# Kernel tuning notes

Hardware: AMD Instinct MI355X
Metric: run time of the kernel (lower is better)

The kernel has to match this reference:

```python
import jax, jax.numpy as jnp
import numpy as np

N_NODES = 100000
N_EDGES = 1250000
D = 64
N_LAYERS = 4


def setup_inputs() -> dict:
    key = jax.random.key(0)
    ks = jax.random.split(key, 6)
    x = jax.random.normal(ks[0], (N_NODES, D), dtype=jnp.float32)
    edge_index = jax.random.randint(ks[1], (2, N_EDGES), 0, N_NODES, dtype=jnp.int64)
    s = 1.0 / np.sqrt(D)
    # PyG SAGEConv per layer: lin_l (applied to aggregated neighbors, with bias)
    # and lin_r (applied to self features, no bias). All layers are 64->64, so stack.
    Wl = jax.random.uniform(ks[2], (N_LAYERS, D, D), dtype=jnp.float32, minval=-s, maxval=s)
    bl = jax.random.uniform(ks[3], (N_LAYERS, D), dtype=jnp.float32, minval=-s, maxval=s)
    Wr = jax.random.uniform(ks[4], (N_LAYERS, D, D), dtype=jnp.float32, minval=-s, maxval=s)
    return {"x": x, "edge_index": edge_index, "Wl": Wl, "bl": bl, "Wr": Wr}


def reference(x, edge_index, Wl, bl, Wr):
    src = edge_index[0]  # message source: x_j
    dst = edge_index[1]  # aggregate at target node
    h = x
    for i in range(N_LAYERS):
        msg = h[src]  # [E, D] irregular gather
        agg = jax.ops.segment_max(msg, dst, num_segments=N_NODES)  # max-pool aggregation
        agg = jnp.where(jnp.isneginf(agg), 0.0, agg)  # empty segments -> 0 (PyG convention)
        h = jax.nn.relu(agg @ Wl[i] + bl[i] + h @ Wr[i])
    return h
```

## Files before the change

kernel.cpp:

```cpp
#include <hip/hip_runtime.h>
#include <hip/hip_fp16.h>
#include <stdint.h>

#define NN 100000
#define NE 1250000
#define DD 64
#define NL 4

#define NPART3 64
#define PSIZE3 1563
#define TILE4 1024
#define NTB ((NE / 4 + TILE4 - 1) / TILE4)
#define SCANA_N (NPART3 * NTB)
#define SRCBITS 17

#define MB2 64
#define L2BLOCKS ((NN + MB2 - 1) / MB2)
#define APAD 136
#define CPADH 72
#define CPADF 68

typedef _Float16 half8 __attribute__((ext_vector_type(8)));
typedef _Float16 half2v __attribute__((ext_vector_type(2)));
typedef float floatx4 __attribute__((ext_vector_type(4)));
typedef int intx4 __attribute__((ext_vector_type(4)));

__device__ __forceinline__ float2 h2f2(unsigned u) {
    __half2 h = *reinterpret_cast<__half2*>(&u);
    return __half22float2(h);
}
__device__ __forceinline__ unsigned f2h2(float a, float b) {
    __half2 h = __floats2half2_rn(a, b);
    return *reinterpret_cast<unsigned*>(&h);
}
__device__ __forceinline__ unsigned umax2(unsigned a, unsigned b) {
    half2v x = *reinterpret_cast<half2v*>(&a);
    half2v y = *reinterpret_cast<half2v*>(&b);
    half2v r = __builtin_elementwise_max(x, y);
    return *reinterpret_cast<unsigned*>(&r);
}

__global__ __launch_bounds__(256) void cast_kernel(const float* __restrict__ x,
                                                   __half* __restrict__ hh) {
    int i = blockIdx.x * 256 + threadIdx.x;
    float4 v = ((const float4*)x)[i];
    uint2 u;
    u.x = f2h2(v.x, v.y);
    u.y = f2h2(v.z, v.w);
    ((uint2*)hh)[i] = u;
}

__global__ __launch_bounds__(256) void countA_kernel(const int* __restrict__ dst,
                                                     int* __restrict__ blockcnt) {
    __shared__ int cnt[NPART3];
    int tid = threadIdx.x;
    if (tid < NPART3) cnt[tid] = 0;
    __syncthreads();
    int b = blockIdx.x;
    #pragma unroll
    for (int r = 0; r < 4; ++r) {
        int i4 = b * TILE4 + r * 256 + tid;
        if (i4 < NE / 4) {
            intx4 d = __builtin_nontemporal_load(&((const intx4*)dst)[i4]);
            atomicAdd(&cnt[(unsigned)d.x / PSIZE3], 1);
            atomicAdd(&cnt[(unsigned)d.y / PSIZE3], 1);
            atomicAdd(&cnt[(unsigned)d.z / PSIZE3], 1);
            atomicAdd(&cnt[(unsigned)d.w / PSIZE3], 1);
        }
    }
    __syncthreads();
    if (tid < NPART3) blockcnt[tid * NTB + b] = cnt[tid];
}

__global__ __launch_bounds__(1024) void scanA_kernel(int* __restrict__ blockcnt) {
    __shared__ int sm[1024];
    int tid = threadIdx.x;
    int base = tid * 20;
    int e[20];
    int s = 0;
    #pragma unroll
    for (int j = 0; j < 20; ++j) {
        e[j] = (base + j < SCANA_N) ? blockcnt[base + j] : 0;
        s += e[j];
    }
    sm[tid] = s;
    __syncthreads();
    for (int off = 1; off < 1024; off <<= 1) {
        int v = (tid >= off) ? sm[tid - off] : 0;
        __syncthreads();
        sm[tid] += v;
        __syncthreads();
    }
    int run = sm[tid] - s;
    #pragma unroll
    for (int j = 0; j < 20; ++j) {
        if (base + j < SCANA_N) {
            blockcnt[base + j] = run;
            run += e[j];
        }
    }
}

__global__ __launch_bounds__(256) void scatterA_kernel(const int* __restrict__ src,
                                                       const int* __restrict__ dst,
                                                       const int* __restrict__ blockcnt,
                                                       int* __restrict__ ebufP) {
    __shared__ int cur[NPART3];
    int tid = threadIdx.x;
    int b = blockIdx.x;
    if (tid < NPART3) cur[tid] = blockcnt[tid * NTB + b];
    __syncthreads();
    #pragma unroll
    for (int r = 0; r < 4; ++r) {
        int i4 = b * TILE4 + r * 256 + tid;
        if (i4 < NE / 4) {
            intx4 d = __builtin_nontemporal_load(&((const intx4*)dst)[i4]);
            intx4 s = __builtin_nontemporal_load(&((const intx4*)src)[i4]);
            int part, p;
            part = (unsigned)d.x / PSIZE3; p = atomicAdd(&cur[part], 1);
            ebufP[p] = ((d.x - part * PSIZE3) << SRCBITS) | s.x;
            part = (unsigned)d.y / PSIZE3; p = atomicAdd(&cur[part], 1);
            ebufP[p] = ((d.y - part * PSIZE3) << SRCBITS) | s.y;
            part = (unsigned)d.z / PSIZE3; p = atomicAdd(&cur[part], 1);
            ebufP[p] = ((d.z - part * PSIZE3) << SRCBITS) | s.z;
            part = (unsigned)d.w / PSIZE3; p = atomicAdd(&cur[part], 1);
            ebufP[p] = ((d.w - part * PSIZE3) << SRCBITS) | s.w;
        }
    }
}

__global__ __launch_bounds__(1024) void fillD_kernel(const int* __restrict__ ebufP,
                                                     const int* __restrict__ blockcnt,
                                                     int* __restrict__ row_start,
                                                     int* __restrict__ csr) {
    __shared__ int cnt[PSIZE3];
    __shared__ int localstart[PSIZE3];
    __shared__ int partial[1024];
    int part = blockIdx.x;
    int tid = threadIdx.x;
    int nbase = part * PSIZE3;
    int base = blockcnt[part * NTB];
    int hi = (part < NPART3 - 1) ? blockcnt[(part + 1) * NTB] : NE;

    for (int j = tid; j < PSIZE3; j += 1024) cnt[j] = 0;
    __syncthreads();

    for (int i = base + tid; i < hi; i += 1024)
        atomicAdd(&cnt[(unsigned)ebufP[i] >> SRCBITS], 1);
    __syncthreads();

    int j0 = tid * 2;
    int e0 = (j0 < PSIZE3) ? cnt[j0] : 0;
    int e1 = (j0 + 1 < PSIZE3) ? cnt[j0 + 1] : 0;
    int s = e0 + e1;
    partial[tid] = s;
    __syncthreads();
    for (int off = 1; off < 1024; off <<= 1) {
        int v = (tid >= off) ? partial[tid - off] : 0;
        __syncthreads();
        partial[tid] += v;
        __syncthreads();
    }
    int run = partial[tid] - s;
    if (j0 < PSIZE3) localstart[j0] = run;
    if (j0 + 1 < PSIZE3) localstart[j0 + 1] = run + e0;
    __syncthreads();

    int nmax = NN - nbase; if (nmax > PSIZE3) nmax = PSIZE3;
    for (int j = tid; j < nmax; j += 1024)
        row_start[nbase + j] = base + localstart[j];
    if (part == NPART3 - 1 && tid == 0) row_start[NN] = NE;

    for (int j = tid; j < PSIZE3; j += 1024) cnt[j] = 0;
    __syncthreads();

    for (int i = base + tid; i < hi; i += 1024) {
        int p = ebufP[i];
        int dl = (unsigned)p >> SRCBITS;
        int local = atomicAdd(&cnt[dl], 1);
        csr[base + localstart[dl] + local] = p & ((1 << SRCBITS) - 1);
    }
}

__global__ __launch_bounds__(256) void agg_kernel(const __half* __restrict__ hh,
                                                  const int* __restrict__ row_start,
                                                  const int* __restrict__ csr,
                                                  __half* __restrict__ aggh) {
    int tid = threadIdx.x;
    int wv = tid >> 6;
    int lane = tid & 63;
    int g = lane >> 3;
    int c8 = (lane & 7) * 8;
    int n = blockIdx.x * 4 + wv;
    int base = row_start[n];
    int cnt = row_start[n + 1] - base;

    if (cnt > 0) {
        int clampi = cnt - 1;
        int pre = (lane <= clampi) ? lane : clampi;
        int idx = csr[base + pre];

        uint4 acc = make_uint4(0xFC00FC00u, 0xFC00FC00u, 0xFC00FC00u, 0xFC00FC00u);
        int kmax = (cnt < 64) ? cnt : 64;
        for (int k = 0; k < kmax; k += 16) {
            int k0 = k + g;
            int k1 = k + g + 8;
            int s0 = __shfl(idx, (k0 <= clampi) ? k0 : clampi, 64);
            int s1 = __shfl(idx, (k1 <= clampi) ? k1 : clampi, 64);
            if (k0 < cnt) {
                uint4 u0 = *(const uint4*)&hh[(size_t)s0 * DD + c8];
                acc.x = umax2(acc.x, u0.x);
                acc.y = umax2(acc.y, u0.y);
                acc.z = umax2(acc.z, u0.z);
                acc.w = umax2(acc.w, u0.w);
            }
            if (k1 < cnt) {
                uint4 u1 = *(const uint4*)&hh[(size_t)s1 * DD + c8];
                acc.x = umax2(acc.x, u1.x);
                acc.y = umax2(acc.y, u1.y);
                acc.z = umax2(acc.z, u1.z);
                acc.w = umax2(acc.w, u1.w);
            }
        }
        for (int k = 64 + g; k < cnt; k += 8) {
            int s = csr[base + k];
            uint4 u = *(const uint4*)&hh[(size_t)s * DD + c8];
            acc.x = umax2(acc.x, u.x);
            acc.y = umax2(acc.y, u.y);
            acc.z = umax2(acc.z, u.z);
            acc.w = umax2(acc.w, u.w);
        }
        #pragma unroll
        for (int off = 8; off <= 32; off <<= 1) {
            acc.x = umax2(acc.x, (unsigned)__shfl_xor((int)acc.x, off, 64));
            acc.y = umax2(acc.y, (unsigned)__shfl_xor((int)acc.y, off, 64));
            acc.z = umax2(acc.z, (unsigned)__shfl_xor((int)acc.z, off, 64));
            acc.w = umax2(acc.w, (unsigned)__shfl_xor((int)acc.w, off, 64));
        }
        if (lane < 8) *(uint4*)&aggh[(size_t)n * DD + c8] = acc;
    } else {
        if (lane < 8) {
            uint4 z = make_uint4(0, 0, 0, 0);
            *(uint4*)&aggh[(size_t)n * DD + c8] = z;
        }
    }
}

__global__ __launch_bounds__(256, 4) void layer_mfma_kernel(
        const __half* __restrict__ aggh,
        __half* __restrict__ hh,
        float* __restrict__ hout,
        const float* __restrict__ Wl,
        const float* __restrict__ bl,
        const float* __restrict__ Wr,
        int last) {
    __shared__ char smem[2 * MB2 * APAD * 2];
    _Float16* a_s  = (_Float16*)smem;
    _Float16* bt_s = (_Float16*)(smem + MB2 * APAD * 2);

    int tid = threadIdx.x;
    int lane = tid & 63;
    int w = tid >> 6;
    int node0 = blockIdx.x * MB2;

    #pragma unroll
    for (int i = 0; i < 4; ++i) {
        int idx = i * 256 + tid;
        int r = idx >> 4;
        int c4 = idx & 15;
        int node = node0 + r; if (node > NN - 1) node = NN - 1;
        const __half* srcp = (c4 < 8) ? (aggh + (size_t)node * DD + c4 * 8)
                                      : (hh + (size_t)node * DD + (c4 - 8) * 8);
        uint4 v = *(const uint4*)srcp;
        *(uint4*)&a_s[r * APAD + c4 * 8] = v;
    }
    {
        int n = tid & 63;
        int kb = tid >> 6;
        #pragma unroll
        for (int kk = 0; kk < 32; ++kk) {
            int k = kb * 32 + kk;
            float wv = (k < 64) ? Wl[k * DD + n] : Wr[(k - 64) * DD + n];
            bt_s[n * APAD + k] = (_Float16)wv;
        }
    }
    __syncthreads();

    floatx4 acc[4];
    #pragma unroll
    for (int nt = 0; nt < 4; ++nt) acc[nt] = (floatx4){0.f, 0.f, 0.f, 0.f};
    int m = lane & 15;
    int q = lane >> 4;

    #pragma unroll
    for (int ks = 0; ks < 4; ++ks) {
        half8 af = *(half8*)&a_s[(w * 16 + m) * APAD + q * 8 + ks * 32];
        #pragma unroll
        for (int nt = 0; nt < 4; ++nt) {
            half8 bf = *(half8*)&bt_s[(nt * 16 + m) * APAD + q * 8 + ks * 32];
            acc[nt] = __builtin_amdgcn_mfma_f32_16x16x32_f16(af, bf, acc[nt], 0, 0, 0);
        }
    }
    __syncthreads();

    _Float16* ch = (_Float16*)smem;
    float*    cf = (float*)(smem + MB2 * CPADH * 2);

    #pragma unroll
    for (int nt = 0; nt < 4; ++nt) {
        int col = nt * 16 + m;
        float b = bl[col];
        #pragma unroll
        for (int r = 0; r < 4; ++r) {
            int rowl = w * 16 + q * 4 + r;
            float o = fmaxf(acc[nt][r] + b, 0.0f);
            ch[rowl * CPADH + col] = (_Float16)o;
            if (last) cf[rowl * CPADF + col] = o;
        }
    }
    __syncthreads();

    #pragma unroll
    for (int i = 0; i < 2; ++i) {
        int idx = i * 256 + tid;
        int r = idx >> 3;
        int c4 = idx & 7;
        int node = node0 + r;
        if (node < NN) {
            uint4 v = *(uint4*)&ch[r * CPADH + c4 * 8];
            *(uint4*)&hh[(size_t)node * DD + c4 * 8] = v;
        }
    }
    if (last) {
        #pragma unroll
        for (int i = 0; i < 4; ++i) {
            int idx = i * 256 + tid;
            int r = idx >> 4;
            int c4 = idx & 15;
            int node = node0 + r;
            if (node < NN) {
                float4 v = *(float4*)&cf[r * CPADF + c4 * 4];
                *(float4*)&hout[(size_t)node * DD + c4 * 4] = v;
            }
        }
    }
}

extern "C" void kernel_launch(void* const* d_in, const int* in_sizes, int n_in,
                              void* d_out, int out_size, void* d_ws, size_t ws_size,
                              hipStream_t stream) {
    const float* x  = (const float*)d_in[0];
    const int*   ei = (const int*)d_in[1];
    const float* Wl = (const float*)d_in[2];
    const float* bl = (const float*)d_in[3];
    const float* Wr = (const float*)d_in[4];
    float* h = (float*)d_out;

    const int* src = ei;
    const int* dst = ei + NE;

    char* ws = (char*)d_ws;
    __half* aggh     = (__half*)ws;  ws += (size_t)NN * DD * sizeof(__half);
    __half* hh       = (__half*)ws;  ws += (size_t)NN * DD * sizeof(__half);
    int* row_start   = (int*)ws;     ws += (size_t)(NN + 16) * sizeof(int);
    int* blockcnt    = (int*)ws;     ws += (size_t)(SCANA_N + 16) * sizeof(int);
    int* csr         = (int*)ws;

    int* ebufP = (int*)aggh;

    cast_kernel<<<(NN * DD / 4) / 256, 256, 0, stream>>>(x, hh);

    countA_kernel<<<NTB, 256, 0, stream>>>(dst, blockcnt);
    scanA_kernel<<<1, 1024, 0, stream>>>(blockcnt);
    scatterA_kernel<<<NTB, 256, 0, stream>>>(src, dst, blockcnt, ebufP);
    fillD_kernel<<<NPART3, 1024, 0, stream>>>(ebufP, blockcnt, row_start, csr);

    for (int l = 0; l < NL; ++l) {
        agg_kernel<<<NN / 4, 256, 0, stream>>>(hh, row_start, csr, aggh);
        layer_mfma_kernel<<<L2BLOCKS, 256, 0, stream>>>(
            aggh, hh, h, Wl + (size_t)l * DD * DD, bl + (size_t)l * DD, Wr + (size_t)l * DD * DD,
            (l == NL - 1) ? 1 : 0);
    }
}
```

Baseline: 317.5 us.

## Fuse max-aggregation gather into the MFMA layer kernel with ping-pong buffers

Removes the separate aggregation kernel: each wave of the layer kernel now gathers and max-reduces neighbor features for 16 nodes directly into shared memory before the MFMA. The fp16 hidden state ping-pongs between two buffers so reads and writes don't race. This cuts the intermediate aggregation buffer's global write and read and one launch per layer. In exchange, each wave handles its 16 nodes one after another, with far fewer blocks in flight, which can hurt latency hiding for the irregular gathers.

```diff
diff --git a/kernel.cpp b/kernel.cpp
--- a/kernel.cpp
+++ b/kernel.cpp
@@ -25,10 +25,6 @@
 typedef float floatx4 __attribute__((ext_vector_type(4)));
 typedef int intx4 __attribute__((ext_vector_type(4)));
 
-__device__ __forceinline__ float2 h2f2(unsigned u) {
-    __half2 h = *reinterpret_cast<__half2*>(&u);
-    return __half22float2(h);
-}
 __device__ __forceinline__ unsigned f2h2(float a, float b) {
     __half2 h = __floats2half2_rn(a, b);
     return *reinterpret_cast<unsigned*>(&h);
@@ -182,74 +178,12 @@
     }
 }
 
-__global__ __launch_bounds__(256) void agg_kernel(const __half* __restrict__ hh,
-                                                  const int* __restrict__ row_start,
-                                                  const int* __restrict__ csr,
-                                                  __half* __restrict__ aggh) {
-    int tid = threadIdx.x;
-    int wv = tid >> 6;
-    int lane = tid & 63;
-    int g = lane >> 3;
-    int c8 = (lane & 7) * 8;
-    int n = blockIdx.x * 4 + wv;
-    int base = row_start[n];
-    int cnt = row_start[n + 1] - base;
-
-    if (cnt > 0) {
-        int clampi = cnt - 1;
-        int pre = (lane <= clampi) ? lane : clampi;
-        int idx = csr[base + pre];
-
-        uint4 acc = make_uint4(0xFC00FC00u, 0xFC00FC00u, 0xFC00FC00u, 0xFC00FC00u);
-        int kmax = (cnt < 64) ? cnt : 64;
-        for (int k = 0; k < kmax; k += 16) {
-            int k0 = k + g;
-            int k1 = k + g + 8;
-            int s0 = __shfl(idx, (k0 <= clampi) ? k0 : clampi, 64);
-            int s1 = __shfl(idx, (k1 <= clampi) ? k1 : clampi, 64);
-            if (k0 < cnt) {
-                uint4 u0 = *(const uint4*)&hh[(size_t)s0 * DD + c8];
-                acc.x = umax2(acc.x, u0.x);
-                acc.y = umax2(acc.y, u0.y);
-                acc.z = umax2(acc.z, u0.z);
-                acc.w = umax2(acc.w, u0.w);
-            }
-            if (k1 < cnt) {
-                uint4 u1 = *(const uint4*)&hh[(size_t)s1 * DD + c8];
-                acc.x = umax2(acc.x, u1.x);
-                acc.y = umax2(acc.y, u1.y);
-                acc.z = umax2(acc.z, u1.z);
-                acc.w = umax2(acc.w, u1.w);
-            }
-        }
-        for (int k = 64 + g; k < cnt; k += 8) {
-            int s = csr[base + k];
-            uint4 u = *(const uint4*)&hh[(size_t)s * DD + c8];
-            acc.x = umax2(acc.x, u.x);
-            acc.y = umax2(acc.y, u.y);
-            acc.z = umax2(acc.z, u.z);
-            acc.w = umax2(acc.w, u.w);
-        }
-        #pragma unroll
-        for (int off = 8; off <= 32; off <<= 1) {
-            acc.x = umax2(acc.x, (unsigned)__shfl_xor((int)acc.x, off, 64));
-            acc.y = umax2(acc.y, (unsigned)__shfl_xor((int)acc.y, off, 64));
-            acc.z = umax2(acc.z, (unsigned)__shfl_xor((int)acc.z, off, 64));
-            acc.w = umax2(acc.w, (unsigned)__shfl_xor((int)acc.w, off, 64));
-        }
-        if (lane < 8) *(uint4*)&aggh[(size_t)n * DD + c8] = acc;
-    } else {
-        if (lane < 8) {
-            uint4 z = make_uint4(0, 0, 0, 0);
-            *(uint4*)&aggh[(size_t)n * DD + c8] = z;
-        }
-    }
-}
-
-__global__ __launch_bounds__(256, 4) void layer_mfma_kernel(
-        const __half* __restrict__ aggh,
-        __half* __restrict__ hh,
-        float* __restrict__ hout,
+__global__ __launch_bounds__(256, 4) void fused_layer_kernel(
+        const __half* __restrict__ hin,
+        __half* __restrict__ hout16,
+        float* __restrict__ houtf,
+        const int* __restrict__ row_start,
+        const int* __restrict__ csr,
         const float* __restrict__ Wl,
         const float* __restrict__ bl,
         const float* __restrict__ Wr,
@@ -263,17 +197,6 @@
     int w = tid >> 6;
     int node0 = blockIdx.x * MB2;
 
-    #pragma unroll
-    for (int i = 0; i < 4; ++i) {
-        int idx = i * 256 + tid;
-        int r = idx >> 4;
-        int c4 = idx & 15;
-        int node = node0 + r; if (node > NN - 1) node = NN - 1;
-        const __half* srcp = (c4 < 8) ? (aggh + (size_t)node * DD + c4 * 8)
-                                      : (hh + (size_t)node * DD + (c4 - 8) * 8);
-        uint4 v = *(const uint4*)srcp;
-        *(uint4*)&a_s[r * APAD + c4 * 8] = v;
-    }
     {
         int n = tid & 63;
         int kb = tid >> 6;
@@ -283,6 +206,68 @@
             float wv = (k < 64) ? Wl[k * DD + n] : Wr[(k - 64) * DD + n];
             bt_s[n * APAD + k] = (_Float16)wv;
         }
+    }
+    #pragma unroll
+    for (int i = 0; i < 2; ++i) {
+        int idx = i * 256 + tid;
+        int r = idx >> 3;
+        int c = idx & 7;
+        int node = node0 + r; if (node > NN - 1) node = NN - 1;
+        *(uint4*)&a_s[r * APAD + DD + c * 8] =
+            *(const uint4*)&hin[(size_t)node * DD + c * 8];
+    }
+
+    int g = lane >> 3;
+    int c8 = (lane & 7) * 8;
+    for (int i = 0; i < 16; ++i) {
+        int r = w * 16 + i;
+        int n = node0 + r; if (n > NN - 1) n = NN - 1;
+        int base = row_start[n];
+        int cnt = row_start[n + 1] - base;
+        uint4 acc = make_uint4(0, 0, 0, 0);
+        if (cnt > 0) {
+            int clampi = cnt - 1;
+            int pre = (lane <= clampi) ? lane : clampi;
+            int idx = csr[base + pre];
+            acc = make_uint4(0xFC00FC00u, 0xFC00FC00u, 0xFC00FC00u, 0xFC00FC00u);
+            int kmax = (cnt < 64) ? cnt : 64;
+            for (int k = 0; k < kmax; k += 16) {
+                int k0 = k + g;
+                int k1 = k + g + 8;
+                int s0 = __shfl(idx, (k0 <= clampi) ? k0 : clampi, 64);
+                int s1 = __shfl(idx, (k1 <= clampi) ? k1 : clampi, 64);
+                if (k0 < cnt) {
+                    uint4 u0 = *(const uint4*)&hin[(size_t)s0 * DD + c8];
+                    acc.x = umax2(acc.x, u0.x);
+                    acc.y = umax2(acc.y, u0.y);
+                    acc.z = umax2(acc.z, u0.z);
+                    acc.w = umax2(acc.w, u0.w);
+                }
+                if (k1 < cnt) {
+                    uint4 u1 = *(const uint4*)&hin[(size_t)s1 * DD + c8];
+                    acc.x = umax2(acc.x, u1.x);
+                    acc.y = umax2(acc.y, u1.y);
+                    acc.z = umax2(acc.z, u1.z);
+                    acc.w = umax2(acc.w, u1.w);
+                }
+            }
+            for (int k = 64 + g; k < cnt; k += 8) {
+                int s = csr[base + k];
+                uint4 u = *(const uint4*)&hin[(size_t)s * DD + c8];
+                acc.x = umax2(acc.x, u.x);
+                acc.y = umax2(acc.y, u.y);
+                acc.z = umax2(acc.z, u.z);
+                acc.w = umax2(acc.w, u.w);
+            }
+            #pragma unroll
+            for (int off = 8; off <= 32; off <<= 1) {
+                acc.x = umax2(acc.x, (unsigned)__shfl_xor((int)acc.x, off, 64));
+                acc.y = umax2(acc.y, (unsigned)__shfl_xor((int)acc.y, off, 64));
+                acc.z = umax2(acc.z, (unsigned)__shfl_xor((int)acc.z, off, 64));
+                acc.w = umax2(acc.w, (unsigned)__shfl_xor((int)acc.w, off, 64));
+            }
+        }
+        if (lane < 8) *(uint4*)&a_s[r * APAD + c8] = acc;
     }
     __syncthreads();
 
@@ -328,7 +313,7 @@
         int node = node0 + r;
         if (node < NN) {
             uint4 v = *(uint4*)&ch[r * CPADH + c4 * 8];
-            *(uint4*)&hh[(size_t)node * DD + c4 * 8] = v;
+            *(uint4*)&hout16[(size_t)node * DD + c4 * 8] = v;
         }
     }
     if (last) {
@@ -340,7 +325,7 @@
             int node = node0 + r;
             if (node < NN) {
                 float4 v = *(float4*)&cf[r * CPADF + c4 * 4];
-                *(float4*)&hout[(size_t)node * DD + c4 * 4] = v;
+                *(float4*)&houtf[(size_t)node * DD + c4 * 4] = v;
             }
         }
     }
@@ -360,15 +345,15 @@
     const int* dst = ei + NE;
 
     char* ws = (char*)d_ws;
-    __half* aggh     = (__half*)ws;  ws += (size_t)NN * DD * sizeof(__half);
-    __half* hh       = (__half*)ws;  ws += (size_t)NN * DD * sizeof(__half);
+    __half* hh0      = (__half*)ws;  ws += (size_t)NN * DD * sizeof(__half);
+    __half* hh1      = (__half*)ws;  ws += (size_t)NN * DD * sizeof(__half);
     int* row_start   = (int*)ws;     ws += (size_t)(NN + 16) * sizeof(int);
     int* blockcnt    = (int*)ws;     ws += (size_t)(SCANA_N + 16) * sizeof(int);
     int* csr         = (int*)ws;
 
-    int* ebufP = (int*)aggh;
-
-    cast_kernel<<<(NN * DD / 4) / 256, 256, 0, stream>>>(x, hh);
+    int* ebufP = (int*)hh1;
+
+    cast_kernel<<<(NN * DD / 4) / 256, 256, 0, stream>>>(x, hh0);
 
     countA_kernel<<<NTB, 256, 0, stream>>>(dst, blockcnt);
     scanA_kernel<<<1, 1024, 0, stream>>>(blockcnt);
@@ -376,9 +361,11 @@
     fillD_kernel<<<NPART3, 1024, 0, stream>>>(ebufP, blockcnt, row_start, csr);
 
     for (int l = 0; l < NL; ++l) {
-        agg_kernel<<<NN / 4, 256, 0, stream>>>(hh, row_start, csr, aggh);
-        layer_mfma_kernel<<<L2BLOCKS, 256, 0, stream>>>(
-            aggh, hh, h, Wl + (size_t)l * DD * DD, bl + (size_t)l * DD, Wr + (size_t)l * DD * DD,
+        const __half* hin = (l & 1) ? hh1 : hh0;
+        __half* hout16    = (l & 1) ? hh0 : hh1;
+        fused_layer_kernel<<<L2BLOCKS, 256, 0, stream>>>(
+            hin, hout16, h, row_start, csr,
+            Wl + (size_t)l * DD * DD, bl + (size_t)l * DD, Wr + (size_t)l * DD * DD,
             (l == NL - 1) ? 1 : 0);
     }
 }
```

Result: slower. 385.8 us (+21.5%).
